# Kernel optimization log

Hardware: AMD Instinct MI355X
Metric: run time of the kernel (lower is better)

The kernel has to match this reference:

```python
import jax, jax.numpy as jnp
import numpy as np

N = 50000      # nodes
E = 800000     # edges
IN_DIM = 512
OUT_DIM = 64
NUM_HEADS = 8
NEG_SLOPE = 0.2


def setup_inputs() -> dict:
    key = jax.random.key(0)
    ks = jax.random.split(key, 8)
    feat = jax.random.normal(ks[0], (N, IN_DIM), dtype=jnp.float32)
    dist = jax.random.uniform(ks[1], (E, NUM_HEADS), dtype=jnp.float32)
    src = jax.random.randint(ks[2], (E,), 0, N, dtype=jnp.int32)
    dst = jax.random.randint(ks[3], (E,), 0, N, dtype=jnp.int32)
    # learned parameters (match torch init scales loosely)
    W = jax.random.normal(ks[4], (NUM_HEADS * OUT_DIM, IN_DIM), dtype=jnp.float32) / np.sqrt(IN_DIM)
    b = jax.random.normal(ks[5], (NUM_HEADS * OUT_DIM,), dtype=jnp.float32) * 0.01
    w_att_src = jax.random.normal(ks[6], (NUM_HEADS, OUT_DIM), dtype=jnp.float32)
    w_att_dst = jax.random.normal(ks[7], (NUM_HEADS, OUT_DIM), dtype=jnp.float32)
    return {"feat": feat, "dist": dist, "src": src, "dst": dst,
            "W": W, "b": b, "w_att_src": w_att_src, "w_att_dst": w_att_dst}


def reference(feat, dist, src, dst, W, b, w_att_src, w_att_dst):
    # Linear + LeakyReLU: [N, H*D]
    h = jax.nn.leaky_relu(feat @ W.T + b, negative_slope=NEG_SLOPE)
    h = h.reshape(N, NUM_HEADS, OUT_DIM)          # [N, H, D]
    # per-node attention logits
    e_src = jnp.sum(h * w_att_src, axis=-1)        # [N, H]
    e_dst = jnp.sum(h * w_att_dst, axis=-1)        # [N, H]
    # gather onto edges (u_add_v) + LeakyReLU
    e = jax.nn.leaky_relu(e_src[src] + e_dst[dst], negative_slope=NEG_SLOPE)  # [E, H]
    # edge_softmax: segment softmax over incoming edges of each dst node
    m = jax.ops.segment_max(e, dst, num_segments=N)      # [N, H]
    ex = jnp.exp(e - m[dst])                             # [E, H]
    s = jax.ops.segment_sum(ex, dst, num_segments=N)     # [N, H]
    a = (ex / s[dst]) * dist                             # [E, H]
    # u_mul_e + sum aggregation
    msg = h[src] * a[:, :, None]                         # [E, H, D]
    out = jax.ops.segment_sum(msg, dst, num_segments=N)  # [N, H, D]
    return out.reshape(N, NUM_HEADS * OUT_DIM)
```

## Files before the change

### kernel.cpp

```cpp
#include <hip/hip_runtime.h>

#define NNODES 50000
#define NEDGES 800000
#define INDIM  512
#define OUTD   512
#define NHEADS 8

typedef float  f32x4  __attribute__((ext_vector_type(4)));
typedef __bf16 bf16x8 __attribute__((ext_vector_type(8)));
typedef __bf16 bf16x4 __attribute__((ext_vector_type(4)));

__device__ __forceinline__ float lrelu(float x) { return x > 0.f ? x : 0.2f * x; }

constexpr int BM = 128, BN = 128, BK = 32, LDA = BK + 8;

__global__ __launch_bounds__(256) void gemm_h(
    const float* __restrict__ feat, const float* __restrict__ W,
    const float* __restrict__ bias, const float* __restrict__ w_s,
    const float* __restrict__ w_d, __bf16* __restrict__ hout,
    float* __restrict__ esrc, float* __restrict__ edst,
    const int* __restrict__ dstv, int* __restrict__ deg)
{
    __shared__ __bf16 As[BM][LDA];
    __shared__ __bf16 Bs[BN][LDA];
    const int row0 = blockIdx.x * BM;
    const int col0 = blockIdx.y * BN;
    const int tid  = threadIdx.x;

    {
        int bid = blockIdx.y * gridDim.x + blockIdx.x;
        int lo = bid * 512, hi = lo + 512;
        if (hi > NEDGES) hi = NEDGES;
        for (int e = lo + tid; e < hi; e += 256)
            atomicAdd(&deg[dstv[e]], 1);
    }

    const int lane = tid & 63;
    const int w    = tid >> 6;
    const int wr   = w >> 1, wc = w & 1;
    const int lr   = lane & 15, kg = lane >> 4;

    f32x4 acc[4][4] = {};

    for (int k0 = 0; k0 < INDIM; k0 += BK) {
        #pragma unroll
        for (int i = 0; i < 4; ++i) {
            int idx = tid + 256 * i;
            int r = idx >> 3, c4 = idx & 7;
            int gr = row0 + r;
            f32x4 v = {0.f, 0.f, 0.f, 0.f};
            if (gr < NNODES) v = *(const f32x4*)(feat + (size_t)gr * INDIM + k0 + c4 * 4);
            bf16x4 bv; bv[0]=(__bf16)v[0]; bv[1]=(__bf16)v[1]; bv[2]=(__bf16)v[2]; bv[3]=(__bf16)v[3];
            *(bf16x4*)&As[r][c4 * 4] = bv;
            f32x4 u = *(const f32x4*)(W + (size_t)(col0 + r) * INDIM + k0 + c4 * 4);
            bf16x4 bu; bu[0]=(__bf16)u[0]; bu[1]=(__bf16)u[1]; bu[2]=(__bf16)u[2]; bu[3]=(__bf16)u[3];
            *(bf16x4*)&Bs[r][c4 * 4] = bu;
        }
        __syncthreads();
        bf16x8 af[4], bf[4];
        #pragma unroll
        for (int mi = 0; mi < 4; ++mi) af[mi] = *(const bf16x8*)&As[wr * 64 + mi * 16 + lr][kg * 8];
        #pragma unroll
        for (int ni = 0; ni < 4; ++ni) bf[ni] = *(const bf16x8*)&Bs[wc * 64 + ni * 16 + lr][kg * 8];
        #pragma unroll
        for (int mi = 0; mi < 4; ++mi)
            #pragma unroll
            for (int ni = 0; ni < 4; ++ni)
                acc[mi][ni] = __builtin_amdgcn_mfma_f32_16x16x32_bf16(af[mi], bf[ni], acc[mi][ni], 0, 0, 0);
        __syncthreads();
    }

    float cb[4], wsv[4], wdv[4];
    #pragma unroll
    for (int ni = 0; ni < 4; ++ni) {
        int c = col0 + wc * 64 + ni * 16 + lr;
        cb[ni]  = bias[c];
        wsv[ni] = w_s[c];
        wdv[ni] = w_d[c];
    }
    const int head = (col0 + wc * 64) >> 6;
    #pragma unroll
    for (int mi = 0; mi < 4; ++mi) {
        #pragma unroll
        for (int reg = 0; reg < 4; ++reg) {
            int r = row0 + wr * 64 + mi * 16 + kg * 4 + reg;
            bool valid = r < NNODES;
            float vs = 0.f, vd = 0.f;
            #pragma unroll
            for (int ni = 0; ni < 4; ++ni) {
                int c = col0 + wc * 64 + ni * 16 + lr;
                float v = acc[mi][ni][reg] + cb[ni];
                v = lrelu(v);
                if (valid) hout[(size_t)r * OUTD + c] = (__bf16)v;
                vs += v * wsv[ni];
                vd += v * wdv[ni];
            }
            #pragma unroll
            for (int m = 1; m < 16; m <<= 1) { vs += __shfl_xor(vs, m); vd += __shfl_xor(vd, m); }
            if (valid && lr == 0) {
                esrc[r * NHEADS + head] = vs;
                edst[r * NHEADS + head] = vd;
            }
        }
    }
}

__global__ __launch_bounds__(256) void scan_bsums(const int* __restrict__ deg, int* __restrict__ bsums)
{
    __shared__ int sd[256];
    int t = threadIdx.x, base = blockIdx.x * 1024, sum = 0;
    #pragma unroll
    for (int i = 0; i < 4; ++i) { int idx = base + t * 4 + i; if (idx < NNODES) sum += deg[idx]; }
    sd[t] = sum; __syncthreads();
    for (int st = 128; st > 0; st >>= 1) { if (t < st) sd[t] += sd[t + st]; __syncthreads(); }
    if (t == 0) bsums[blockIdx.x] = sd[0];
}

__global__ void scan_partials(int* __restrict__ bsums)
{
    int l = threadIdx.x;
    int orig = (l < 49) ? bsums[l] : 0;
    int v = orig;
    #pragma unroll
    for (int d = 1; d < 64; d <<= 1) { int u = __shfl_up(v, d); if (l >= d) v += u; }
    if (l < 49) bsums[l] = v - orig;
}

__global__ __launch_bounds__(256) void scan_final(
    const int* __restrict__ deg, const int* __restrict__ bsums,
    int* __restrict__ offs, int* __restrict__ cursor)
{
    __shared__ int sd[256];
    int t = threadIdx.x, base = blockIdx.x * 1024;
    int v[4]; int sum = 0;
    #pragma unroll
    for (int i = 0; i < 4; ++i) { int idx = base + t * 4 + i; v[i] = (idx < NNODES) ? deg[idx] : 0; sum += v[i]; }
    sd[t] = sum; __syncthreads();
    int val = sum;
    for (int st = 1; st < 256; st <<= 1) {
        int add = (t >= st) ? sd[t - st] : 0;
        __syncthreads();
        val += add; sd[t] = val;
        __syncthreads();
    }
    int run = bsums[blockIdx.x] + (val - sum);
    #pragma unroll
    for (int i = 0; i < 4; ++i) {
        int idx = base + t * 4 + i;
        if (idx < NNODES) { offs[idx] = run; cursor[idx] = run; }
        run += v[i];
    }
    if (blockIdx.x == 0 && t == 0) offs[NNODES] = NEDGES;
}

__global__ void scatter_k(const int* __restrict__ dstv, const int* __restrict__ src,
                          int* __restrict__ cursor, int2* __restrict__ perm)
{
    int e = blockIdx.x * blockDim.x + threadIdx.x;
    if (e < NEDGES) {
        int pos = atomicAdd(&cursor[dstv[e]], 1);
        perm[pos] = make_int2(src[e], e);
    }
}

__global__ __launch_bounds__(256) void agg_k(
    const int* __restrict__ offs, const int2* __restrict__ perm,
    const float* __restrict__ esrc, const float* __restrict__ edst,
    const float* __restrict__ dist, const __bf16* __restrict__ hmat,
    float* __restrict__ out)
{
    int node = blockIdx.x * 4 + (threadIdx.x >> 6);
    int lane = threadIdx.x & 63;
    if (node >= NNODES) return;
    const int head = lane >> 3;
    const float edv = edst[(size_t)node * NHEADS + head];
    int beg = offs[node], end = offs[node + 1];
    float denom = 0.f;
    float acc[8] = {};

    int pos = beg;
    for (; pos + 4 <= end; pos += 4) {
        int2 a0 = perm[pos], a1 = perm[pos + 1], a2 = perm[pos + 2], a3 = perm[pos + 3];
        float es0 = esrc[(size_t)a0.x * NHEADS + head];
        float es1 = esrc[(size_t)a1.x * NHEADS + head];
        float es2 = esrc[(size_t)a2.x * NHEADS + head];
        float es3 = esrc[(size_t)a3.x * NHEADS + head];
        float di0 = dist[(size_t)a0.y * NHEADS + head];
        float di1 = dist[(size_t)a1.y * NHEADS + head];
        float di2 = dist[(size_t)a2.y * NHEADS + head];
        float di3 = dist[(size_t)a3.y * NHEADS + head];
        bf16x8 h0 = *(const bf16x8*)(hmat + (size_t)a0.x * OUTD + lane * 8);
        bf16x8 h1 = *(const bf16x8*)(hmat + (size_t)a1.x * OUTD + lane * 8);
        bf16x8 h2 = *(const bf16x8*)(hmat + (size_t)a2.x * OUTD + lane * 8);
        bf16x8 h3 = *(const bf16x8*)(hmat + (size_t)a3.x * OUTD + lane * 8);
        float ex0 = __expf(lrelu(es0 + edv));
        float ex1 = __expf(lrelu(es1 + edv));
        float ex2 = __expf(lrelu(es2 + edv));
        float ex3 = __expf(lrelu(es3 + edv));
        denom += (ex0 + ex1) + (ex2 + ex3);
        float w0 = ex0 * di0, w1 = ex1 * di1, w2 = ex2 * di2, w3 = ex3 * di3;
        #pragma unroll
        for (int j = 0; j < 8; ++j)
            acc[j] += (w0 * (float)h0[j] + w1 * (float)h1[j])
                    + (w2 * (float)h2[j] + w3 * (float)h3[j]);
    }
    for (; pos < end; ++pos) {
        int2 a0 = perm[pos];
        float es0 = esrc[(size_t)a0.x * NHEADS + head];
        float di0 = dist[(size_t)a0.y * NHEADS + head];
        bf16x8 h0 = *(const bf16x8*)(hmat + (size_t)a0.x * OUTD + lane * 8);
        float ex0 = __expf(lrelu(es0 + edv));
        denom += ex0;
        float w0 = ex0 * di0;
        #pragma unroll
        for (int j = 0; j < 8; ++j) acc[j] += w0 * (float)h0[j];
    }

    float sinv = denom > 0.f ? 1.f / denom : 0.f;
    f32x4 o0 = {acc[0] * sinv, acc[1] * sinv, acc[2] * sinv, acc[3] * sinv};
    f32x4 o1 = {acc[4] * sinv, acc[5] * sinv, acc[6] * sinv, acc[7] * sinv};
    *(f32x4*)(out + (size_t)node * OUTD + lane * 8)     = o0;
    *(f32x4*)(out + (size_t)node * OUTD + lane * 8 + 4) = o1;
}

extern "C" void kernel_launch(void* const* d_in, const int* in_sizes, int n_in,
                              void* d_out, int out_size, void* d_ws, size_t ws_size,
                              hipStream_t stream)
{
    const float* feat = (const float*)d_in[0];
    const float* dist = (const float*)d_in[1];
    const int*   src  = (const int*)d_in[2];
    const int*   dstv = (const int*)d_in[3];
    const float* W    = (const float*)d_in[4];
    const float* bias = (const float*)d_in[5];
    const float* w_s  = (const float*)d_in[6];
    const float* w_d  = (const float*)d_in[7];
    float* out = (float*)d_out;

    char* wsb = (char*)d_ws;
    size_t off = 0;
    auto alloc = [&](size_t bytes) -> char* {
        char* r = wsb + off;
        off = (off + bytes + 255) & ~(size_t)255;
        return r;
    };
    __bf16* hmat  = (__bf16*)alloc((size_t)NNODES * OUTD * 2);
    float*  esrc  = (float*)alloc((size_t)NNODES * NHEADS * 4);
    float*  edst  = (float*)alloc((size_t)NNODES * NHEADS * 4);
    int*    deg   = (int*)alloc((size_t)NNODES * 4);
    int*    offs  = (int*)alloc((size_t)(NNODES + 1) * 4);
    int*    cursor= (int*)alloc((size_t)NNODES * 4);
    int2*   perm  = (int2*)alloc((size_t)NEDGES * 8);
    int*    bsums = (int*)alloc(64 * 4);

    hipMemsetAsync(deg, 0, (size_t)NNODES * 4, stream);

    gemm_h<<<dim3((NNODES + BM - 1) / BM, OUTD / BN), 256, 0, stream>>>(
        feat, W, bias, w_s, w_d, hmat, esrc, edst, dstv, deg);

    scan_bsums<<<49, 256, 0, stream>>>(deg, bsums);
    scan_partials<<<1, 64, 0, stream>>>(bsums);
    scan_final<<<49, 256, 0, stream>>>(deg, bsums, offs, cursor);
    scatter_k<<<(NEDGES + 255) / 256, 256, 0, stream>>>(dstv, src, cursor, perm);

    agg_k<<<(NNODES + 3) / 4, 256, 0, stream>>>(offs, perm, esrc, edst, dist, hmat, out);
}
```

Baseline: 524.3 us.

## Pre-convert inputs to bf16 and stage GEMM tiles via direct global-to-LDS loads

```diff
diff --git a/kernel.cpp b/kernel.cpp
--- a/kernel.cpp
+++ b/kernel.cpp
@@ -8,23 +8,37 @@
 
 typedef float  f32x4  __attribute__((ext_vector_type(4)));
 typedef __bf16 bf16x8 __attribute__((ext_vector_type(8)));
-typedef __bf16 bf16x4 __attribute__((ext_vector_type(4)));
 
 __device__ __forceinline__ float lrelu(float x) { return x > 0.f ? x : 0.2f * x; }
 
-constexpr int BM = 128, BN = 128, BK = 32, LDA = BK + 8;
+__global__ __launch_bounds__(256) void cvt_k(const float* __restrict__ f,
+                                             __bf16* __restrict__ o, int n8)
+{
+    int i = blockIdx.x * 256 + threadIdx.x;
+    int stride = gridDim.x * 256;
+    for (; i < n8; i += stride) {
+        f32x4 a = *(const f32x4*)(f + (size_t)i * 8);
+        f32x4 b = *(const f32x4*)(f + (size_t)i * 8 + 4);
+        bf16x8 v;
+        v[0]=(__bf16)a[0]; v[1]=(__bf16)a[1]; v[2]=(__bf16)a[2]; v[3]=(__bf16)a[3];
+        v[4]=(__bf16)b[0]; v[5]=(__bf16)b[1]; v[6]=(__bf16)b[2]; v[7]=(__bf16)b[3];
+        *(bf16x8*)(o + (size_t)i * 8) = v;
+    }
+}
+
+constexpr int BM = 128, BN = 128;
 
 __global__ __launch_bounds__(256) void gemm_h(
-    const float* __restrict__ feat, const float* __restrict__ W,
+    const __bf16* __restrict__ featb, const __bf16* __restrict__ Wb,
     const float* __restrict__ bias, const float* __restrict__ w_s,
     const float* __restrict__ w_d, __bf16* __restrict__ hout,
     float* __restrict__ esrc, float* __restrict__ edst,
     const int* __restrict__ dstv, int* __restrict__ deg)
 {
-    __shared__ __bf16 As[BM][LDA];
-    __shared__ __bf16 Bs[BN][LDA];
-    const int row0 = blockIdx.x * BM;
-    const int col0 = blockIdx.y * BN;
+    __shared__ __bf16 As[BM][64];
+    __shared__ __bf16 Bs[BN][64];
+    const int col0 = blockIdx.x * BN;
+    const int row0 = blockIdx.y * BM;
     const int tid  = threadIdx.x;
 
     {
@@ -40,33 +54,48 @@
     const int wr   = w >> 1, wc = w & 1;
     const int lr   = lane & 15, kg = lane >> 4;
 
+    int srcA[4], srcB[4];
+    #pragma unroll
+    for (int i = 0; i < 4; ++i) {
+        int p = tid + 256 * i;
+        int r = p >> 3, ps = p & 7, sub = ps ^ (r & 7);
+        int gra = row0 + r; if (gra > NNODES - 1) gra = NNODES - 1;
+        srcA[i] = gra * INDIM + sub * 8;
+        srcB[i] = (col0 + r) * INDIM + sub * 8;
+    }
+
     f32x4 acc[4][4] = {};
 
-    for (int k0 = 0; k0 < INDIM; k0 += BK) {
+    for (int k0 = 0; k0 < INDIM; k0 += 64) {
         #pragma unroll
         for (int i = 0; i < 4; ++i) {
-            int idx = tid + 256 * i;
-            int r = idx >> 3, c4 = idx & 7;
-            int gr = row0 + r;
-            f32x4 v = {0.f, 0.f, 0.f, 0.f};
-            if (gr < NNODES) v = *(const f32x4*)(feat + (size_t)gr * INDIM + k0 + c4 * 4);
-            bf16x4 bv; bv[0]=(__bf16)v[0]; bv[1]=(__bf16)v[1]; bv[2]=(__bf16)v[2]; bv[3]=(__bf16)v[3];
-            *(bf16x4*)&As[r][c4 * 4] = bv;
-            f32x4 u = *(const f32x4*)(W + (size_t)(col0 + r) * INDIM + k0 + c4 * 4);
-            bf16x4 bu; bu[0]=(__bf16)u[0]; bu[1]=(__bf16)u[1]; bu[2]=(__bf16)u[2]; bu[3]=(__bf16)u[3];
-            *(bf16x4*)&Bs[r][c4 * 4] = bu;
+            int p = tid + 256 * i;
+            __builtin_amdgcn_global_load_lds(
+                (const __attribute__((address_space(1))) void*)(featb + srcA[i] + k0),
+                (__attribute__((address_space(3))) void*)((char*)&As[0][0] + p * 16),
+                16, 0, 0);
+            __builtin_amdgcn_global_load_lds(
+                (const __attribute__((address_space(1))) void*)(Wb + srcB[i] + k0),
+                (__attribute__((address_space(3))) void*)((char*)&Bs[0][0] + p * 16),
+                16, 0, 0);
         }
         __syncthreads();
-        bf16x8 af[4], bf[4];
-        #pragma unroll
-        for (int mi = 0; mi < 4; ++mi) af[mi] = *(const bf16x8*)&As[wr * 64 + mi * 16 + lr][kg * 8];
-        #pragma unroll
-        for (int ni = 0; ni < 4; ++ni) bf[ni] = *(const bf16x8*)&Bs[wc * 64 + ni * 16 + lr][kg * 8];
-        #pragma unroll
-        for (int mi = 0; mi < 4; ++mi)
+        #pragma unroll
+        for (int ks = 0; ks < 2; ++ks) {
+            bf16x8 af[4], bf[4];
+            const int pc = ((ks * 4 + kg) ^ (lr & 7)) * 16;
+            #pragma unroll
+            for (int mi = 0; mi < 4; ++mi)
+                af[mi] = *(const bf16x8*)((const char*)&As[0][0] + (wr*64 + mi*16 + lr) * 128 + pc);
             #pragma unroll
             for (int ni = 0; ni < 4; ++ni)
-                acc[mi][ni] = __builtin_amdgcn_mfma_f32_16x16x32_bf16(af[mi], bf[ni], acc[mi][ni], 0, 0, 0);
+                bf[ni] = *(const bf16x8*)((const char*)&Bs[0][0] + (wc*64 + ni*16 + lr) * 128 + pc);
+            #pragma unroll
+            for (int mi = 0; mi < 4; ++mi)
+                #pragma unroll
+                for (int ni = 0; ni < 4; ++ni)
+                    acc[mi][ni] = __builtin_amdgcn_mfma_f32_16x16x32_bf16(af[mi], bf[ni], acc[mi][ni], 0, 0, 0);
+        }
         __syncthreads();
     }
 
@@ -245,6 +274,8 @@
         return r;
     };
     __bf16* hmat  = (__bf16*)alloc((size_t)NNODES * OUTD * 2);
+    __bf16* featb = (__bf16*)alloc((size_t)NNODES * INDIM * 2);
+    __bf16* Wb    = (__bf16*)alloc((size_t)OUTD * INDIM * 2);
     float*  esrc  = (float*)alloc((size_t)NNODES * NHEADS * 4);
     float*  edst  = (float*)alloc((size_t)NNODES * NHEADS * 4);
     int*    deg   = (int*)alloc((size_t)NNODES * 4);
@@ -255,8 +286,11 @@
 
     hipMemsetAsync(deg, 0, (size_t)NNODES * 4, stream);
 
-    gemm_h<<<dim3((NNODES + BM - 1) / BM, OUTD / BN), 256, 0, stream>>>(
-        feat, W, bias, w_s, w_d, hmat, esrc, edst, dstv, deg);
+    cvt_k<<<2048, 256, 0, stream>>>(feat, featb, NNODES * INDIM / 8);
+    cvt_k<<<128, 256, 0, stream>>>(W, Wb, OUTD * INDIM / 8);
+
+    gemm_h<<<dim3(OUTD / BN, (NNODES + BM - 1) / BM), 256, 0, stream>>>(
+        featb, Wb, bias, w_s, w_d, hmat, esrc, edst, dstv, deg);
 
     scan_bsums<<<49, 256, 0, stream>>>(deg, bsums);
     scan_partials<<<1, 64, 0, stream>>>(bsums);
```

Result: faster. 484.5 us (-7.6%).
